# Kernel tuning notes

Measured on AMD Instinct MI355X. Metric: run time of the kernel, lower is better.

The kernel has to match this reference:

```python
import jax, jax.numpy as jnp
import numpy as np

B, K, D, E, V, T = 128, 49, 512, 256, 10000, 20


def setup_inputs() -> dict:
    key = jax.random.key(0)
    ks = jax.random.split(key, 20)
    rn = lambda k, shape, s=0.02: jax.random.normal(k, shape, jnp.float32) * s
    lengths = jnp.sort(jax.random.randint(ks[3], (B,), 1, T + 1))[::-1]
    lengths = lengths.at[0].set(T)  # max(lengths) == T, sorted descending
    return {
        "spatial": jax.random.normal(ks[0], (B, K, D), jnp.float32),
        "global_feats": jax.random.normal(ks[1], (B, D), jnp.float32),
        "captions": jax.random.randint(ks[2], (B, T), 0, V),
        "lengths": lengths,
        "emb": rn(ks[4], (V, E), 0.05),
        "W_init_h": rn(ks[5], (D, D)), "b_init_h": jnp.zeros((D,), jnp.float32),
        "W_init_m": rn(ks[6], (D, D)), "b_init_m": jnp.zeros((D,), jnp.float32),
        "W_ih": rn(ks[7], (4 * D, E + D)), "b_ih": jnp.zeros((4 * D,), jnp.float32),
        "W_hh": rn(ks[8], (4 * D, D)), "b_hh": jnp.zeros((4 * D,), jnp.float32),
        "Wv": rn(ks[9], (K, D)), "bv": jnp.zeros((K,), jnp.float32),
        "Wg": rn(ks[10], (K, D)), "bg": jnp.zeros((K,), jnp.float32),
        "wh": rn(ks[11], (1, K)), "bh_att": jnp.zeros((1,), jnp.float32),
        "Wp": rn(ks[12], (V, D)), "bp": jnp.zeros((V,), jnp.float32),
    }


def reference(spatial, global_feats, captions, lengths, emb,
              W_init_h, b_init_h, W_init_m, b_init_m,
              W_ih, b_ih, W_hh, b_hh,
              Wv, bv, Wg, bg, wh, bh_att, Wp, bp):
    # initialize_state
    h0 = global_feats @ W_init_h.T + b_init_h  # [B,D]
    m0 = global_feats @ W_init_m.T + b_init_m
    emb_seq = emb[captions]                     # [B,T,E]
    V_proj = spatial @ Wv.T + bv                # [B,K,K] (attn hidden = k), loop-invariant

    def step(carry, xs):
        h, m = carry
        w, t = xs                               # w: [B,E]
        active = (lengths > t)[:, None]         # masked equivalent of shrinking batch
        x = jnp.concatenate([w, global_feats], axis=1)  # [B,E+D]
        gates = x @ W_ih.T + b_ih + h @ W_hh.T + b_hh   # [B,4D]
        i, f, g, o = jnp.split(gates, 4, axis=1)        # torch LSTMCell gate order
        i, f, o = jax.nn.sigmoid(i), jax.nn.sigmoid(f), jax.nn.sigmoid(o)
        g = jnp.tanh(g)
        m_new = f * m + i * g
        h_new = o * jnp.tanh(m_new)
        h = jnp.where(active, h_new, h)
        m = jnp.where(active, m_new, m)
        # spatial attention: z = w_h^T tanh(W_v V + W_g h)
        z = jnp.tanh(V_proj + (h @ Wg.T + bg)[:, None, :]) @ wh[0] + bh_att[0]  # [B,K]
        alpha = jax.nn.softmax(z, axis=1)
        c = jnp.einsum('bk,bkd->bd', alpha, spatial)
        logit = (c + h) @ Wp.T + bp             # [B,V]
        logit = jnp.where(active, logit, 0.0)
        return (h, m), logit

    xs = (emb_seq.transpose(1, 0, 2), jnp.arange(T))
    (_, _), logits = jax.lax.scan(step, (h0, m0), xs)
    return logits.transpose(1, 0, 2)            # [B,T,V]
```

## Files before the change

kernel.cpp:

```cpp
#include <hip/hip_runtime.h>
#include <hip/hip_bf16.h>
#include <math.h>

typedef __bf16 bf16;
typedef __bf16 v8bf __attribute__((ext_vector_type(8)));
typedef __bf16 v4bfv __attribute__((ext_vector_type(4)));
typedef float  v4f  __attribute__((ext_vector_type(4)));

#define B_   128
#define KK_  49
#define D_   512
#define E_   256
#define V_   10000
#define T_   20
#define NG_  2048
#define XK_  768
#define VPAD 10112
#define NP_  128

#define GLOAD_LDS16(gp, lp) \
    __builtin_amdgcn_global_load_lds((const __attribute__((address_space(1))) void*)(gp), \
                                     (__attribute__((address_space(3))) void*)(lp), 16, 0, 0)

__device__ inline v4bfv cvt4(float4 v) {
    v4bfv o; o[0] = (bf16)v.x; o[1] = (bf16)v.y; o[2] = (bf16)v.z; o[3] = (bf16)v.w;
    return o;
}

__global__ void prep_kernel(
    const float* __restrict__ spatial, const float* __restrict__ gfeat,
    const int* __restrict__ caps, const float* __restrict__ emb,
    const float* __restrict__ W_init_h, const float* __restrict__ W_init_m,
    const float* __restrict__ W_ih, const float* __restrict__ b_ih,
    const float* __restrict__ W_hh, const float* __restrict__ b_hh,
    const float* __restrict__ Wv, const float* __restrict__ bv,
    const float* __restrict__ Wg, const float* __restrict__ bg,
    const float* __restrict__ Wp,
    bf16* __restrict__ Wp_b, bf16* __restrict__ Whh_b, bf16* __restrict__ Wih_b,
    bf16* __restrict__ Xin_b, bf16* __restrict__ Sp_b,
    bf16* __restrict__ Wv_b, bf16* __restrict__ Wg_b,
    bf16* __restrict__ Winh_b, bf16* __restrict__ Winm_b, bf16* __restrict__ Gf_b,
    float* __restrict__ bias_comb, float* __restrict__ bv_pad, float* __restrict__ bg_pad)
{
    const int stride = gridDim.x * blockDim.x;
    const int tid0 = blockIdx.x * blockDim.x + threadIdx.x;
    const float4 z4 = make_float4(0.f, 0.f, 0.f, 0.f);

    for (int i4 = tid0; i4 < VPAD * D_ / 4; i4 += stride) {
        int row = i4 >> 7;
        float4 v = (row < V_) ? ((const float4*)Wp)[i4] : z4;
        ((v4bfv*)Wp_b)[i4] = cvt4(v);
    }
    for (int i4 = tid0; i4 < NG_ * D_ / 4; i4 += stride)
        ((v4bfv*)Whh_b)[i4] = cvt4(((const float4*)W_hh)[i4]);
    for (int i4 = tid0; i4 < NG_ * XK_ / 4; i4 += stride)
        ((v4bfv*)Wih_b)[i4] = cvt4(((const float4*)W_ih)[i4]);
    for (int i4 = tid0; i4 < T_ * B_ * XK_ / 4; i4 += stride) {
        int r = i4 / (XK_ / 4), c4 = i4 - r * (XK_ / 4);
        int c = c4 * 4;
        int t = r >> 7, b = r & 127;
        float4 v;
        if (c < E_) v = *(const float4*)&emb[(long)caps[b * T_ + t] * E_ + c];
        else        v = *(const float4*)&gfeat[(long)b * D_ + (c - E_)];
        ((v4bfv*)Xin_b)[i4] = cvt4(v);
    }
    for (int i4 = tid0; i4 < B_ * KK_ * D_ / 4; i4 += stride)
        ((v4bfv*)Sp_b)[i4] = cvt4(((const float4*)spatial)[i4]);
    for (int i4 = tid0; i4 < NP_ * D_ / 4; i4 += stride) {
        int row = i4 >> 7;
        ((v4bfv*)Wv_b)[i4] = cvt4((row < KK_) ? ((const float4*)Wv)[i4] : z4);
        ((v4bfv*)Wg_b)[i4] = cvt4((row < KK_) ? ((const float4*)Wg)[i4] : z4);
    }
    for (int i4 = tid0; i4 < D_ * D_ / 4; i4 += stride) {
        ((v4bfv*)Winh_b)[i4] = cvt4(((const float4*)W_init_h)[i4]);
        ((v4bfv*)Winm_b)[i4] = cvt4(((const float4*)W_init_m)[i4]);
    }
    for (int i4 = tid0; i4 < B_ * D_ / 4; i4 += stride)
        ((v4bfv*)Gf_b)[i4] = cvt4(((const float4*)gfeat)[i4]);
    for (int i = tid0; i < NG_; i += stride) bias_comb[i] = b_ih[i] + b_hh[i];
    for (int i = tid0; i < NP_; i += stride) {
        bv_pad[i] = (i < KK_) ? bv[i] : 0.f;
        bg_pad[i] = (i < KK_) ? bg[i] : 0.f;
    }
}

template <int OUTMODE>
__global__ __launch_bounds__(256) void gemm_bt(
    const bf16* __restrict__ A, const bf16* __restrict__ Bm,
    const float* __restrict__ bias, void* __restrict__ Cout,
    int M, int N, int K, int out_stride, int n_real, const int* __restrict__ lengths)
{
    __shared__ bf16 As[128 * 32];
    __shared__ bf16 Bs[128 * 32];
    const int m0 = blockIdx.x * 128, n0 = blockIdx.y * 128;
    const int tid = threadIdx.x;
    const int w = tid >> 6, l = tid & 63;
    const int wm = (w >> 1) * 64, wn = (w & 1) * 64;
    const int lr = l & 15, lq = l >> 4;

    v4f acc[4][4] = {};

    for (int k0 = 0; k0 < K; k0 += 32) {
        __syncthreads();
        #pragma unroll
        for (int c = 0; c < 2; c++) {
            int u = c * 256 + tid;
            int row = u >> 2, kc = (u & 3) * 8;
            int u0 = c * 256 + (tid & ~63);
            GLOAD_LDS16(&A[(long)(m0 + row) * K + k0 + kc], &As[u0 * 8]);
            GLOAD_LDS16(&Bm[(long)(n0 + row) * K + k0 + kc], &Bs[u0 * 8]);
        }
        __syncthreads();
        v8bf af[4], bfv[4];
        #pragma unroll
        for (int s = 0; s < 4; s++) {
            af[s]  = *(const v8bf*)&As[(wm + s * 16 + lr) * 32 + lq * 8];
            bfv[s] = *(const v8bf*)&Bs[(wn + s * 16 + lr) * 32 + lq * 8];
        }
        #pragma unroll
        for (int i = 0; i < 4; i++)
            #pragma unroll
            for (int j = 0; j < 4; j++)
                acc[i][j] = __builtin_amdgcn_mfma_f32_16x16x32_bf16(af[i], bfv[j], acc[i][j], 0, 0, 0);
    }

    #pragma unroll
    for (int i = 0; i < 4; i++)
        #pragma unroll
        for (int j = 0; j < 4; j++)
            #pragma unroll
            for (int r = 0; r < 4; r++) {
                int m = m0 + wm + i * 16 + lq * 4 + r;
                int n = n0 + wn + j * 16 + lr;
                float v = acc[i][j][r];
                if (OUTMODE == 2) {
                    if (n < n_real) {
                        int t = m % T_, b = m / T_;
                        float o = (t < lengths[b]) ? (v + bias[n]) : 0.f;
                        ((float*)Cout)[(long)m * out_stride + n] = o;
                    }
                } else if (OUTMODE == 1) {
                    ((bf16*)Cout)[(long)m * out_stride + n] = (bf16)(v + bias[n]);
                } else {
                    ((float*)Cout)[(long)m * out_stride + n] = v + bias[n];
                }
            }
}

__global__ __launch_bounds__(256) void step_kernel(
    const bf16* __restrict__ Hprev, bf16* __restrict__ Hnext,
    const bf16* __restrict__ Whh_b, const float* __restrict__ Xpre_t,
    float* __restrict__ mbuf, const int* __restrict__ lengths, int t)
{
    const int b0 = blockIdx.x * 16;
    const int j0 = blockIdx.y * 16;
    const int tid = threadIdx.x;
    const int w = tid >> 6, l = tid & 63;
    const int lr = l & 15, lq = l >> 4;
    __shared__ float g4[4][16][16];

    v4f acc = {};
    const bf16* Arow = Hprev + (long)(b0 + lr) * D_;
    const bf16* Brow = Whh_b + (long)(w * D_ + j0 + lr) * D_;

    #pragma unroll 4
    for (int kk = 0; kk < D_; kk += 32) {
        v8bf af  = *(const v8bf*)&Arow[kk + lq * 8];
        v8bf bfv = *(const v8bf*)&Brow[kk + lq * 8];
        acc = __builtin_amdgcn_mfma_f32_16x16x32_bf16(af, bfv, acc, 0, 0, 0);
    }
    #pragma unroll
    for (int r = 0; r < 4; r++)
        g4[w][lq * 4 + r][lr] = acc[r];
    __syncthreads();

    const int bi = tid >> 4, j = tid & 15;
    const int bgl = b0 + bi, jg = j0 + j;
    const float* xp = Xpre_t + (long)bgl * NG_ + jg;
    float gi = g4[0][bi][j] + xp[0];
    float gf = g4[1][bi][j] + xp[D_];
    float gc = g4[2][bi][j] + xp[2 * D_];
    float go = g4[3][bi][j] + xp[3 * D_];
    gi = 1.f / (1.f + expf(-gi));
    gf = 1.f / (1.f + expf(-gf));
    gc = tanhf(gc);
    go = 1.f / (1.f + expf(-go));
    long idx = (long)bgl * D_ + jg;
    float m_old = mbuf[idx];
    float h_old = (float)Hprev[idx];
    bool active = t < lengths[bgl];
    float m_new = gf * m_old + gi * gc;
    float h_new = go * tanhf(m_new);
    mbuf[idx] = active ? m_new : m_old;
    Hnext[idx] = (bf16)(active ? h_new : h_old);
}

__global__ __launch_bounds__(256) void attn_kernel(
    const bf16* __restrict__ Hb16, const float* __restrict__ g_all,
    const float* __restrict__ Vproj, const float* __restrict__ wh,
    const float* __restrict__ bh_att, const float* __restrict__ spatial,
    bf16* __restrict__ ctx)
{
    const int w = threadIdx.x >> 6, l = threadIdx.x & 63;
    const int b = blockIdx.x / 5, tg = blockIdx.x % 5;
    const int t = tg * 4 + w;
    const int r = t * 128 + b;
    __shared__ float sg[4][64], sal[4][64], swh[64];

    if (w == 0) swh[l] = (l < KK_) ? wh[l] : 0.f;
    sg[w][l] = (l < KK_) ? g_all[(long)r * NP_ + l] : 0.f;
    __syncthreads();

    float z = -1e30f;
    if (l < KK_) {
        const float* vp = Vproj + (long)(b * KK_ + l) * NP_;
        float a = 0.f;
        for (int j = 0; j < KK_; j++)
            a += swh[j] * tanhf(vp[j] + sg[w][j]);
        z = a + bh_att[0];
    }
    float mx = z;
    #pragma unroll
    for (int o = 32; o > 0; o >>= 1) mx = fmaxf(mx, __shfl_xor(mx, o));
    float e = (l < KK_) ? expf(z - mx) : 0.f;
    float sm = e;
    #pragma unroll
    for (int o = 32; o > 0; o >>= 1) sm += __shfl_xor(sm, o);
    sal[w][l] = e / sm;
    __syncthreads();

    const bf16* hrow = Hb16 + (long)(t + 1) * B_ * D_ + (long)b * D_;
    const float* sp = spatial + (long)b * KK_ * D_;
    bf16* crow = ctx + (long)(b * T_ + t) * D_;
    for (int d = l; d < D_; d += 64) {
        float c = 0.f;
        for (int k = 0; k < KK_; k++)
            c += sal[w][k] * sp[k * D_ + d];
        crow[d] = (bf16)(c + (float)hrow[d]);
    }
}

extern "C" void kernel_launch(void* const* d_in, const int* in_sizes, int n_in,
                              void* d_out, int out_size, void* d_ws, size_t ws_size,
                              hipStream_t stream)
{
    const float* spatial  = (const float*)d_in[0];
    const float* gfeat    = (const float*)d_in[1];
    const int*   caps     = (const int*)d_in[2];
    const int*   lengths  = (const int*)d_in[3];
    const float* emb      = (const float*)d_in[4];
    const float* W_init_h = (const float*)d_in[5];
    const float* b_init_h = (const float*)d_in[6];
    const float* W_init_m = (const float*)d_in[7];
    const float* b_init_m = (const float*)d_in[8];
    const float* W_ih     = (const float*)d_in[9];
    const float* b_ih     = (const float*)d_in[10];
    const float* W_hh     = (const float*)d_in[11];
    const float* b_hh     = (const float*)d_in[12];
    const float* Wv       = (const float*)d_in[13];
    const float* bv       = (const float*)d_in[14];
    const float* Wg       = (const float*)d_in[15];
    const float* bg       = (const float*)d_in[16];
    const float* wh       = (const float*)d_in[17];
    const float* bh_att   = (const float*)d_in[18];
    const float* Wp       = (const float*)d_in[19];
    const float* bp       = (const float*)d_in[20];
    float* out = (float*)d_out;

    char* ws = (char*)d_ws;
    size_t off = 0;
    auto alloc = [&](size_t bytes) -> void* {
        off = (off + 255) & ~(size_t)255;
        void* p = ws + off;
        off += bytes;
        return p;
    };

    bf16* Wp_b   = (bf16*)alloc((size_t)VPAD * D_ * 2);
    bf16* Whh_b  = (bf16*)alloc((size_t)NG_ * D_ * 2);
    bf16* Wih_b  = (bf16*)alloc((size_t)NG_ * XK_ * 2);
    bf16* Xin_b  = (bf16*)alloc((size_t)T_ * B_ * XK_ * 2);
    bf16* Sp_b   = (bf16*)alloc((size_t)B_ * KK_ * D_ * 2);
    bf16* Wv_b   = (bf16*)alloc((size_t)NP_ * D_ * 2);
    bf16* Wg_b   = (bf16*)alloc((size_t)NP_ * D_ * 2);
    bf16* Winh_b = (bf16*)alloc((size_t)D_ * D_ * 2);
    bf16* Winm_b = (bf16*)alloc((size_t)D_ * D_ * 2);
    bf16* Gf_b   = (bf16*)alloc((size_t)B_ * D_ * 2);
    float* bias_comb = (float*)alloc(NG_ * 4);
    float* bv_pad    = (float*)alloc(NP_ * 4);
    float* bg_pad    = (float*)alloc(NP_ * 4);
    bf16* Hb16   = (bf16*)alloc((size_t)(T_ + 1) * B_ * D_ * 2);
    float* mbuf  = (float*)alloc((size_t)B_ * D_ * 4);
    float* Xpre  = (float*)alloc((size_t)T_ * B_ * NG_ * 4);
    float* VprojW = (float*)alloc((size_t)B_ * KK_ * NP_ * 4);
    float* g_allW = (float*)alloc((size_t)T_ * B_ * NP_ * 4);
    bf16* ctx    = (bf16*)alloc((size_t)T_ * B_ * D_ * 2);

    prep_kernel<<<1024, 256, 0, stream>>>(
        spatial, gfeat, caps, emb, W_init_h, W_init_m, W_ih, b_ih, W_hh, b_hh,
        Wv, bv, Wg, bg, Wp,
        Wp_b, Whh_b, Wih_b, Xin_b, Sp_b, Wv_b, Wg_b, Winh_b, Winm_b, Gf_b,
        bias_comb, bv_pad, bg_pad);

    gemm_bt<1><<<dim3(1, 4), 256, 0, stream>>>(Gf_b, Winh_b, b_init_h, Hb16,
                                               B_, D_, D_, D_, 0, nullptr);
    gemm_bt<0><<<dim3(1, 4), 256, 0, stream>>>(Gf_b, Winm_b, b_init_m, mbuf,
                                               B_, D_, D_, D_, 0, nullptr);

    gemm_bt<0><<<dim3((B_ * KK_) / 128, 1), 256, 0, stream>>>(
        Sp_b, Wv_b, bv_pad, VprojW, B_ * KK_, NP_, D_, NP_, 0, nullptr);

    gemm_bt<0><<<dim3((T_ * B_) / 128, NG_ / 128), 256, 0, stream>>>(
        Xin_b, Wih_b, bias_comb, Xpre, T_ * B_, NG_, XK_, NG_, 0, nullptr);

    for (int t = 0; t < T_; t++) {
        step_kernel<<<dim3(8, 32), 256, 0, stream>>>(
            Hb16 + (size_t)t * B_ * D_, Hb16 + (size_t)(t + 1) * B_ * D_,
            Whh_b, Xpre + (size_t)t * B_ * NG_, mbuf, lengths, t);
    }

    gemm_bt<0><<<dim3((T_ * B_) / 128, 1), 256, 0, stream>>>(
        Hb16 + (size_t)B_ * D_, Wg_b, bg_pad, g_allW, T_ * B_, NP_, D_, NP_, 0, nullptr);

    attn_kernel<<<B_ * 5, 256, 0, stream>>>(Hb16, g_allW, VprojW, wh, bh_att,
                                            spatial, ctx);

    gemm_bt<2><<<dim3((T_ * B_) / 128, VPAD / 128), 256, 0, stream>>>(
        ctx, Wp_b, bp, out, T_ * B_, VPAD, D_, V_, V_, lengths);
}
```

Baseline: 490.3 us.

## Fuse LSTM time loop into persistent cooperative kernel with LDS-resident W_hh

Replaces the 20 per-step launches of the LSTM recurrence with one cooperative persistent kernel. Each block keeps most of its W_hh slice in LDS and holds h and m in registers, synchronising across timesteps with grid.sync. This removes per-step launch overhead and repeated weight reloads, at the cost of grid-wide barriers. It also merges the two init-state GEMMs into one launch and doubles the GEMM k-step to 64, which halves the number of barriers per tile but doubles LDS use per block.

```diff
diff --git a/kernel.cpp b/kernel.cpp
--- a/kernel.cpp
+++ b/kernel.cpp
@@ -1,6 +1,9 @@
 #include <hip/hip_runtime.h>
 #include <hip/hip_bf16.h>
+#include <hip/hip_cooperative_groups.h>
 #include <math.h>
+
+namespace cg = cooperative_groups;
 
 typedef __bf16 bf16;
 typedef __bf16 v8bf __attribute__((ext_vector_type(8)));
@@ -30,7 +33,8 @@
 __global__ void prep_kernel(
     const float* __restrict__ spatial, const float* __restrict__ gfeat,
     const int* __restrict__ caps, const float* __restrict__ emb,
-    const float* __restrict__ W_init_h, const float* __restrict__ W_init_m,
+    const float* __restrict__ W_init_h, const float* __restrict__ b_init_h,
+    const float* __restrict__ W_init_m, const float* __restrict__ b_init_m,
     const float* __restrict__ W_ih, const float* __restrict__ b_ih,
     const float* __restrict__ W_hh, const float* __restrict__ b_hh,
     const float* __restrict__ Wv, const float* __restrict__ bv,
@@ -39,8 +43,9 @@
     bf16* __restrict__ Wp_b, bf16* __restrict__ Whh_b, bf16* __restrict__ Wih_b,
     bf16* __restrict__ Xin_b, bf16* __restrict__ Sp_b,
     bf16* __restrict__ Wv_b, bf16* __restrict__ Wg_b,
-    bf16* __restrict__ Winh_b, bf16* __restrict__ Winm_b, bf16* __restrict__ Gf_b,
-    float* __restrict__ bias_comb, float* __restrict__ bv_pad, float* __restrict__ bg_pad)
+    bf16* __restrict__ Winit2_b, bf16* __restrict__ Gf_b,
+    float* __restrict__ bias_comb, float* __restrict__ bias_init,
+    float* __restrict__ bv_pad, float* __restrict__ bg_pad)
 {
     const int stride = gridDim.x * blockDim.x;
     const int tid0 = blockIdx.x * blockDim.x + threadIdx.x;
@@ -71,13 +76,17 @@
         ((v4bfv*)Wv_b)[i4] = cvt4((row < KK_) ? ((const float4*)Wv)[i4] : z4);
         ((v4bfv*)Wg_b)[i4] = cvt4((row < KK_) ? ((const float4*)Wg)[i4] : z4);
     }
-    for (int i4 = tid0; i4 < D_ * D_ / 4; i4 += stride) {
-        ((v4bfv*)Winh_b)[i4] = cvt4(((const float4*)W_init_h)[i4]);
-        ((v4bfv*)Winm_b)[i4] = cvt4(((const float4*)W_init_m)[i4]);
+    for (int i4 = tid0; i4 < 2 * D_ * D_ / 4; i4 += stride) {
+        int row = i4 >> 7;
+        float4 v = (row < D_) ? ((const float4*)W_init_h)[i4]
+                              : ((const float4*)W_init_m)[i4 - D_ * (D_ / 4)];
+        ((v4bfv*)Winit2_b)[i4] = cvt4(v);
     }
     for (int i4 = tid0; i4 < B_ * D_ / 4; i4 += stride)
         ((v4bfv*)Gf_b)[i4] = cvt4(((const float4*)gfeat)[i4]);
     for (int i = tid0; i < NG_; i += stride) bias_comb[i] = b_ih[i] + b_hh[i];
+    for (int i = tid0; i < 2 * D_; i += stride)
+        bias_init[i] = (i < D_) ? b_init_h[i] : b_init_m[i - D_];
     for (int i = tid0; i < NP_; i += stride) {
         bv_pad[i] = (i < KK_) ? bv[i] : 0.f;
         bg_pad[i] = (i < KK_) ? bg[i] : 0.f;
@@ -87,11 +96,11 @@
 template <int OUTMODE>
 __global__ __launch_bounds__(256) void gemm_bt(
     const bf16* __restrict__ A, const bf16* __restrict__ Bm,
-    const float* __restrict__ bias, void* __restrict__ Cout,
+    const float* __restrict__ bias, void* __restrict__ Cout, void* __restrict__ Cout2,
     int M, int N, int K, int out_stride, int n_real, const int* __restrict__ lengths)
 {
-    __shared__ bf16 As[128 * 32];
-    __shared__ bf16 Bs[128 * 32];
+    __shared__ bf16 As[2 * 128 * 32];
+    __shared__ bf16 Bs[2 * 128 * 32];
     const int m0 = blockIdx.x * 128, n0 = blockIdx.y * 128;
     const int tid = threadIdx.x;
     const int w = tid >> 6, l = tid & 63;
@@ -100,28 +109,32 @@
 
     v4f acc[4][4] = {};
 
-    for (int k0 = 0; k0 < K; k0 += 32) {
+    for (int k0 = 0; k0 < K; k0 += 64) {
         __syncthreads();
         #pragma unroll
-        for (int c = 0; c < 2; c++) {
+        for (int c = 0; c < 4; c++) {
             int u = c * 256 + tid;
-            int row = u >> 2, kc = (u & 3) * 8;
+            int h = u >> 9, v = u & 511;
+            int row = v >> 2, kc = (v & 3) * 8;
             int u0 = c * 256 + (tid & ~63);
-            GLOAD_LDS16(&A[(long)(m0 + row) * K + k0 + kc], &As[u0 * 8]);
-            GLOAD_LDS16(&Bm[(long)(n0 + row) * K + k0 + kc], &Bs[u0 * 8]);
+            GLOAD_LDS16(&A[(long)(m0 + row) * K + k0 + h * 32 + kc], &As[u0 * 8]);
+            GLOAD_LDS16(&Bm[(long)(n0 + row) * K + k0 + h * 32 + kc], &Bs[u0 * 8]);
         }
         __syncthreads();
-        v8bf af[4], bfv[4];
-        #pragma unroll
-        for (int s = 0; s < 4; s++) {
-            af[s]  = *(const v8bf*)&As[(wm + s * 16 + lr) * 32 + lq * 8];
-            bfv[s] = *(const v8bf*)&Bs[(wn + s * 16 + lr) * 32 + lq * 8];
+        #pragma unroll
+        for (int h = 0; h < 2; h++) {
+            v8bf af[4], bfv[4];
+            #pragma unroll
+            for (int s = 0; s < 4; s++) {
+                af[s]  = *(const v8bf*)&As[h * 4096 + (wm + s * 16 + lr) * 32 + lq * 8];
+                bfv[s] = *(const v8bf*)&Bs[h * 4096 + (wn + s * 16 + lr) * 32 + lq * 8];
+            }
+            #pragma unroll
+            for (int i = 0; i < 4; i++)
+                #pragma unroll
+                for (int j = 0; j < 4; j++)
+                    acc[i][j] = __builtin_amdgcn_mfma_f32_16x16x32_bf16(af[i], bfv[j], acc[i][j], 0, 0, 0);
         }
-        #pragma unroll
-        for (int i = 0; i < 4; i++)
-            #pragma unroll
-            for (int j = 0; j < 4; j++)
-                acc[i][j] = __builtin_amdgcn_mfma_f32_16x16x32_bf16(af[i], bfv[j], acc[i][j], 0, 0, 0);
     }
 
     #pragma unroll
@@ -139,6 +152,9 @@
                         float o = (t < lengths[b]) ? (v + bias[n]) : 0.f;
                         ((float*)Cout)[(long)m * out_stride + n] = o;
                     }
+                } else if (OUTMODE == 3) {
+                    if (n < D_) ((bf16*)Cout)[(long)m * D_ + n] = (bf16)(v + bias[n]);
+                    else ((float*)Cout2)[(long)m * D_ + n - D_] = v + bias[n];
                 } else if (OUTMODE == 1) {
                     ((bf16*)Cout)[(long)m * out_stride + n] = (bf16)(v + bias[n]);
                 } else {
@@ -147,52 +163,77 @@
             }
 }
 
-__global__ __launch_bounds__(256) void step_kernel(
-    const bf16* __restrict__ Hprev, bf16* __restrict__ Hnext,
-    const bf16* __restrict__ Whh_b, const float* __restrict__ Xpre_t,
-    float* __restrict__ mbuf, const int* __restrict__ lengths, int t)
-{
-    const int b0 = blockIdx.x * 16;
-    const int j0 = blockIdx.y * 16;
+__global__ __launch_bounds__(256) void lstm_fused(
+    bf16* __restrict__ Hb16, const bf16* __restrict__ Whh_b,
+    const float* __restrict__ Xpre, const float* __restrict__ mbuf,
+    const int* __restrict__ lengths)
+{
+    cg::grid_group gg = cg::this_grid();
+    const int blk = blockIdx.x;
+    const int bt = blk & 7, jt = blk >> 3;
+    const int b0 = bt * 16, j0 = jt * 16;
     const int tid = threadIdx.x;
     const int w = tid >> 6, l = tid & 63;
     const int lr = l & 15, lq = l >> 4;
+
+    __shared__ bf16 Bl[14 * 64 * 32];
     __shared__ float g4[4][16][16];
 
-    v4f acc = {};
-    const bf16* Arow = Hprev + (long)(b0 + lr) * D_;
-    const bf16* Brow = Whh_b + (long)(w * D_ + j0 + lr) * D_;
-
-    #pragma unroll 4
-    for (int kk = 0; kk < D_; kk += 32) {
-        v8bf af  = *(const v8bf*)&Arow[kk + lq * 8];
-        v8bf bfv = *(const v8bf*)&Brow[kk + lq * 8];
-        acc = __builtin_amdgcn_mfma_f32_16x16x32_bf16(af, bfv, acc, 0, 0, 0);
-    }
-    #pragma unroll
-    for (int r = 0; r < 4; r++)
-        g4[w][lq * 4 + r][lr] = acc[r];
+    for (int c = tid; c < 14 * 256; c += 256) {
+        int p = c >> 8, q = c & 255;
+        int r = q >> 2, kc = (q & 3) * 8;
+        int gate = r >> 4, jr = r & 15;
+        ((int4*)Bl)[c] = *(const int4*)&Whh_b[(long)(gate * D_ + j0 + jr) * D_ + p * 32 + kc];
+    }
+    const bf16* wrow = Whh_b + (long)(w * D_ + j0 + lr) * D_;
+    v8bf bv14 = *(const v8bf*)&wrow[14 * 32 + lq * 8];
+    v8bf bv15 = *(const v8bf*)&wrow[15 * 32 + lq * 8];
+
+    const int bi = tid >> 4, jj = tid & 15;
+    const int bg = b0 + bi, jg = j0 + jj;
+    const long hidx = (long)bg * D_ + jg;
+    float m_st = mbuf[hidx];
+    float h_st = (float)Hb16[hidx];
+    const int len = lengths[bg];
     __syncthreads();
 
-    const int bi = tid >> 4, j = tid & 15;
-    const int bgl = b0 + bi, jg = j0 + j;
-    const float* xp = Xpre_t + (long)bgl * NG_ + jg;
-    float gi = g4[0][bi][j] + xp[0];
-    float gf = g4[1][bi][j] + xp[D_];
-    float gc = g4[2][bi][j] + xp[2 * D_];
-    float go = g4[3][bi][j] + xp[3 * D_];
-    gi = 1.f / (1.f + expf(-gi));
-    gf = 1.f / (1.f + expf(-gf));
-    gc = tanhf(gc);
-    go = 1.f / (1.f + expf(-go));
-    long idx = (long)bgl * D_ + jg;
-    float m_old = mbuf[idx];
-    float h_old = (float)Hprev[idx];
-    bool active = t < lengths[bgl];
-    float m_new = gf * m_old + gi * gc;
-    float h_new = go * tanhf(m_new);
-    mbuf[idx] = active ? m_new : m_old;
-    Hnext[idx] = (bf16)(active ? h_new : h_old);
+    for (int t = 0; t < T_; t++) {
+        const bf16* Arow = Hb16 + (long)t * B_ * D_ + (long)(b0 + lr) * D_;
+        v8bf af[16];
+        #pragma unroll
+        for (int p = 0; p < 16; p++)
+            af[p] = *(const v8bf*)&Arow[p * 32 + lq * 8];
+        v4f acc = {};
+        #pragma unroll
+        for (int p = 0; p < 14; p++) {
+            v8bf bfv = *(const v8bf*)&Bl[p * 2048 + (w * 16 + lr) * 32 + lq * 8];
+            acc = __builtin_amdgcn_mfma_f32_16x16x32_bf16(af[p], bfv, acc, 0, 0, 0);
+        }
+        acc = __builtin_amdgcn_mfma_f32_16x16x32_bf16(af[14], bv14, acc, 0, 0, 0);
+        acc = __builtin_amdgcn_mfma_f32_16x16x32_bf16(af[15], bv15, acc, 0, 0, 0);
+        #pragma unroll
+        for (int r = 0; r < 4; r++)
+            g4[w][lq * 4 + r][lr] = acc[r];
+        __syncthreads();
+
+        const float* xp = Xpre + (long)t * B_ * NG_ + (long)bg * NG_ + jg;
+        float gi = g4[0][bi][jj] + xp[0];
+        float gf = g4[1][bi][jj] + xp[D_];
+        float gc = g4[2][bi][jj] + xp[2 * D_];
+        float go = g4[3][bi][jj] + xp[3 * D_];
+        gi = 1.f / (1.f + expf(-gi));
+        gf = 1.f / (1.f + expf(-gf));
+        gc = tanhf(gc);
+        go = 1.f / (1.f + expf(-go));
+        float m_new = gf * m_st + gi * gc;
+        float h_new = go * tanhf(m_new);
+        bool active = t < len;
+        m_st = active ? m_new : m_st;
+        h_st = active ? h_new : h_st;
+        Hb16[(long)(t + 1) * B_ * D_ + hidx] = (bf16)h_st;
+        __threadfence();
+        gg.sync();
+    }
 }
 
 __global__ __launch_bounds__(256) void attn_kernel(
@@ -276,55 +317,54 @@
         return p;
     };
 
-    bf16* Wp_b   = (bf16*)alloc((size_t)VPAD * D_ * 2);
-    bf16* Whh_b  = (bf16*)alloc((size_t)NG_ * D_ * 2);
-    bf16* Wih_b  = (bf16*)alloc((size_t)NG_ * XK_ * 2);
-    bf16* Xin_b  = (bf16*)alloc((size_t)T_ * B_ * XK_ * 2);
-    bf16* Sp_b   = (bf16*)alloc((size_t)B_ * KK_ * D_ * 2);
-    bf16* Wv_b   = (bf16*)alloc((size_t)NP_ * D_ * 2);
-    bf16* Wg_b   = (bf16*)alloc((size_t)NP_ * D_ * 2);
-    bf16* Winh_b = (bf16*)alloc((size_t)D_ * D_ * 2);
-    bf16* Winm_b = (bf16*)alloc((size_t)D_ * D_ * 2);
-    bf16* Gf_b   = (bf16*)alloc((size_t)B_ * D_ * 2);
+    bf16* Wp_b    = (bf16*)alloc((size_t)VPAD * D_ * 2);
+    bf16* Whh_b   = (bf16*)alloc((size_t)NG_ * D_ * 2);
+    bf16* Wih_b   = (bf16*)alloc((size_t)NG_ * XK_ * 2);
+    bf16* Xin_b   = (bf16*)alloc((size_t)T_ * B_ * XK_ * 2);
+    bf16* Sp_b    = (bf16*)alloc((size_t)B_ * KK_ * D_ * 2);
+    bf16* Wv_b    = (bf16*)alloc((size_t)NP_ * D_ * 2);
+    bf16* Wg_b    = (bf16*)alloc((size_t)NP_ * D_ * 2);
+    bf16* Winit2_b= (bf16*)alloc((size_t)2 * D_ * D_ * 2);
+    bf16* Gf_b    = (bf16*)alloc((size_t)B_ * D_ * 2);
     float* bias_comb = (float*)alloc(NG_ * 4);
+    float* bias_init = (float*)alloc(2 * D_ * 4);
     float* bv_pad    = (float*)alloc(NP_ * 4);
     float* bg_pad    = (float*)alloc(NP_ * 4);
-    bf16* Hb16   = (bf16*)alloc((size_t)(T_ + 1) * B_ * D_ * 2);
-    float* mbuf  = (float*)alloc((size_t)B_ * D_ * 4);
-    float* Xpre  = (float*)alloc((size_t)T_ * B_ * NG_ * 4);
+    bf16* Hb16    = (bf16*)alloc((size_t)(T_ + 1) * B_ * D_ * 2);
+    float* mbuf   = (float*)alloc((size_t)B_ * D_ * 4);
+    float* Xpre   = (float*)alloc((size_t)T_ * B_ * NG_ * 4);
     float* VprojW = (float*)alloc((size_t)B_ * KK_ * NP_ * 4);
     float* g_allW = (float*)alloc((size_t)T_ * B_ * NP_ * 4);
-    bf16* ctx    = (bf16*)alloc((size_t)T_ * B_ * D_ * 2);
+    bf16* ctx     = (bf16*)alloc((size_t)T_ * B_ * D_ * 2);
 
     prep_kernel<<<1024, 256, 0, stream>>>(
-        spatial, gfeat, caps, emb, W_init_h, W_init_m, W_ih, b_ih, W_hh, b_hh,
-        Wv, bv, Wg, bg, Wp,
-        Wp_b, Whh_b, Wih_b, Xin_b, Sp_b, Wv_b, Wg_b, Winh_b, Winm_b, Gf_b,
-        bias_comb, bv_pad, bg_pad);
-
-    gemm_bt<1><<<dim3(1, 4), 256, 0, stream>>>(Gf_b, Winh_b, b_init_h, Hb16,
-                                               B_, D_, D_, D_, 0, nullptr);
-    gemm_bt<0><<<dim3(1, 4), 256, 0, stream>>>(Gf_b, Winm_b, b_init_m, mbuf,
-                                               B_, D_, D_, D_, 0, nullptr);
+        spatial, gfeat, caps, emb, W_init_h, b_init_h, W_init_m, b_init_m,
+        W_ih, b_ih, W_hh, b_hh, Wv, bv, Wg, bg, Wp,
+        Wp_b, Whh_b, Wih_b, Xin_b, Sp_b, Wv_b, Wg_b, Winit2_b, Gf_b,
+        bias_comb, bias_init, bv_pad, bg_pad);
+
+    gemm_bt<3><<<dim3(1, 8), 256, 0, stream>>>(Gf_b, Winit2_b, bias_init,
+                                               Hb16, mbuf, B_, 2 * D_, D_, 0, 0, nullptr);
 
     gemm_bt<0><<<dim3((B_ * KK_) / 128, 1), 256, 0, stream>>>(
-        Sp_b, Wv_b, bv_pad, VprojW, B_ * KK_, NP_, D_, NP_, 0, nullptr);
+        Sp_b, Wv_b, bv_pad, VprojW, nullptr, B_ * KK_, NP_, D_, NP_, 0, nullptr);
 
     gemm_bt<0><<<dim3((T_ * B_) / 128, NG_ / 128), 256, 0, stream>>>(
-        Xin_b, Wih_b, bias_comb, Xpre, T_ * B_, NG_, XK_, NG_, 0, nullptr);
-
-    for (int t = 0; t < T_; t++) {
-        step_kernel<<<dim3(8, 32), 256, 0, stream>>>(
-            Hb16 + (size_t)t * B_ * D_, Hb16 + (size_t)(t + 1) * B_ * D_,
-            Whh_b, Xpre + (size_t)t * B_ * NG_, mbuf, lengths, t);
+        Xin_b, Wih_b, bias_comb, Xpre, nullptr, T_ * B_, NG_, XK_, NG_, 0, nullptr);
+
+    {
+        void* args[] = { (void*)&Hb16, (void*)&Whh_b, (void*)&Xpre,
+                         (void*)&mbuf, (void*)&lengths };
+        hipLaunchCooperativeKernel((void*)lstm_fused, dim3(256), dim3(256),
+                                   args, 0, stream);
     }
 
     gemm_bt<0><<<dim3((T_ * B_) / 128, 1), 256, 0, stream>>>(
-        Hb16 + (size_t)B_ * D_, Wg_b, bg_pad, g_allW, T_ * B_, NP_, D_, NP_, 0, nullptr);
+        Hb16 + (size_t)B_ * D_, Wg_b, bg_pad, g_allW, nullptr, T_ * B_, NP_, D_, NP_, 0, nullptr);
 
     attn_kernel<<<B_ * 5, 256, 0, stream>>>(Hb16, g_allW, VprojW, wh, bh_att,
                                             spatial, ctx);
 
     gemm_bt<2><<<dim3((T_ * B_) / 128, VPAD / 128), 256, 0, stream>>>(
-        ctx, Wp_b, bp, out, T_ * B_, VPAD, D_, V_, V_, lengths);
-}
+        ctx, Wp_b, bp, out, nullptr, T_ * B_, VPAD, D_, V_, V_, lengths);
+}
```

After: 1.464 ms. +198.5%, slower.
